# Kernel tuning notes

Hardware: AMD Instinct MI355X
Metric: run time of the kernel (lower is better)

The kernel has to match this reference:

```python
import jax, jax.numpy as jnp
import numpy as np

D_MODEL = 256
NHEAD = 8
HEAD_DIM = D_MODEL // NHEAD
LN_EPS = 1e-5
NEG_INF = -1e30  # finite large-negative; avoids NaN rows while matching masked softmax


def setup_inputs() -> dict:
    key = jax.random.key(0)
    ks = jax.random.split(key, 9)
    B, Q, HW, D = 8, 100, 16384, D_MODEL
    s = 0.02
    return {
        "query": jax.random.normal(ks[0], (B, Q, D), jnp.float32),
        "key_value": jax.random.normal(ks[1], (B, HW, D), jnp.float32),
        "attn_mask": jax.random.randint(ks[2], (B * NHEAD, Q, HW), 0, 2) == 1,  # True = attend
        "in_proj_weight": jax.random.normal(ks[3], (3 * D, D), jnp.float32) * s,
        "in_proj_bias": jax.random.normal(ks[4], (3 * D,), jnp.float32) * s,
        "out_proj_weight": jax.random.normal(ks[5], (D, D), jnp.float32) * s,
        "out_proj_bias": jax.random.normal(ks[6], (D,), jnp.float32) * s,
        "ln_weight": jnp.ones((D,), jnp.float32),
        "ln_bias": jnp.zeros((D,), jnp.float32),
    }


def _mha_masked(query, key_value, attn_mask, in_proj_weight, in_proj_bias,
                out_proj_weight, out_proj_bias):
    B, Q, D = query.shape
    HW = key_value.shape[1]
    Wq, Wk, Wv = jnp.split(in_proj_weight, 3, axis=0)
    bq, bk, bv = jnp.split(in_proj_bias, 3, axis=0)
    q = (query @ Wq.T + bq).reshape(B, Q, NHEAD, HEAD_DIM)
    k = (key_value @ Wk.T + bk).reshape(B, HW, NHEAD, HEAD_DIM)
    v = (key_value @ Wv.T + bv).reshape(B, HW, NHEAD, HEAD_DIM)
    scale = 1.0 / np.sqrt(HEAD_DIM).astype(np.float32)
    scores = jnp.einsum("bqhd,bkhd->bhqk", q, k) * scale  # (B, H, Q, HW)
    attend = attn_mask.reshape(B, NHEAD, Q, HW)  # True = attend
    scores = jnp.where(attend, scores, NEG_INF)
    probs = jax.nn.softmax(scores, axis=-1)
    ctx = jnp.einsum("bhqk,bkhd->bqhd", probs, v).reshape(B, Q, D)
    return ctx @ out_proj_weight.T + out_proj_bias


def reference(query, key_value, attn_mask, in_proj_weight, in_proj_bias,
              out_proj_weight, out_proj_bias, ln_weight, ln_bias):
    attn_out = _mha_masked(query, key_value, attn_mask, in_proj_weight,
                           in_proj_bias, out_proj_weight, out_proj_bias)
    x = query + attn_out  # dropout p=0.0 is identity
    mu = jnp.mean(x, axis=-1, keepdims=True)
    var = jnp.mean(jnp.square(x - mu), axis=-1, keepdims=True)
    return (x - mu) * jax.lax.rsqrt(var + LN_EPS) * ln_weight + ln_bias
```

## Files before the change

kernel.cpp:

```cpp
#include <hip/hip_runtime.h>
#include <stdint.h>

#define BB   8
#define NH   8
#define QQ   100
#define HWK  16384
#define DM   256
#define HD   32
#define QP   112
#define MT   7
#define NPART 64
#define SCALE2 0.2550602534365564f

typedef short bf16x8 __attribute__((ext_vector_type(8)));
typedef float f32x4  __attribute__((ext_vector_type(4)));
typedef unsigned short u16;
typedef unsigned int   u32;
typedef unsigned long long u64;

__device__ __forceinline__ u16 f2bf(float f) {
  u32 u = __builtin_bit_cast(u32, f);
  u += 0x7fffu + ((u >> 16) & 1u);
  return (u16)(u >> 16);
}
__device__ __forceinline__ u16 f2bf_ru(float f) {
  return (u16)((__builtin_bit_cast(u32, f) + 0x8000u) >> 16);
}
__device__ __forceinline__ u32 pack2rn(float lo, float hi) {
  u32 a = __builtin_bit_cast(u32, lo) + 0x8000u;
  u32 b = __builtin_bit_cast(u32, hi) + 0x8000u;
  return __builtin_amdgcn_perm(b, a, 0x07060302u);
}
__device__ __forceinline__ float bf_lo(u32 u) {
  return __builtin_bit_cast(float, u << 16);
}
__device__ __forceinline__ float bf_hi(u32 u) {
  return __builtin_bit_cast(float, u & 0xffff0000u);
}
__device__ __forceinline__ float fast_exp2(float x) {
#if __has_builtin(__builtin_amdgcn_exp2f)
  return __builtin_amdgcn_exp2f(x);
#else
  return exp2f(x);
#endif
}

__global__ __launch_bounds__(256) void wconv_kernel(
    const float* __restrict__ W, u16* __restrict__ wbf) {
  const int i = (blockIdx.x * 256 + threadIdx.x) * 4;
  const float4 w = *(const float4*)(W + 256 * DM + i);
  u32* dst = (u32*)(wbf + i);
  dst[0] = pack2rn(w.x, w.y);
  dst[1] = pack2rn(w.z, w.w);
}

__global__ __launch_bounds__(256) void proj_q_kernel(
    const float* __restrict__ query, const float* __restrict__ W,
    const float* __restrict__ bias, u16* __restrict__ q_bf) {
  __shared__ float xrow[DM];
  const int bq = blockIdx.x;
  const int b = bq / QQ, qi = bq % QQ;
  const int tid = threadIdx.x;
  if (tid < 64)
    ((float4*)xrow)[tid] = ((const float4*)(query + (size_t)bq * DM))[tid];
  __syncthreads();
  const int j = tid;
  float acc = bias[j];
  const float4* wr = (const float4*)(W + (size_t)j * DM);
  #pragma unroll 8
  for (int c = 0; c < 64; ++c) {
    float4 w = wr[c];
    float4 x = ((const float4*)xrow)[c];
    acc += w.x * x.x + w.y * x.y + w.z * x.z + w.w * x.w;
  }
  acc *= SCALE2;
  const int h = j >> 5, d = j & 31;
  q_bf[(((size_t)(b * NH + h)) * QQ + qi) * HD + d] = f2bf(acc);
}

__global__ __launch_bounds__(256) void proj_kv_kernel(
    const float* __restrict__ kv, const u16* __restrict__ wbf,
    const float* __restrict__ bias, u16* __restrict__ k_bf,
    u16* __restrict__ v_t) {
  __shared__ u16 Tl[4][5120];
  const int rb = blockIdx.x;
  const size_t m0 = (size_t)rb * 64;
  const int tid = threadIdx.x, lane = tid & 63, wid = tid >> 6;
  const int lane15 = lane & 15, quad = lane >> 4;
  const int jw = wid * 128;

  f32x4 acc[4][8];
  #pragma unroll
  for (int mi = 0; mi < 4; ++mi)
    #pragma unroll
    for (int ni = 0; ni < 8; ++ni) acc[mi][ni] = (f32x4){0.f, 0.f, 0.f, 0.f};

  for (int ks = 0; ks < 8; ++ks) {
    bf16x8 afr[4];
    #pragma unroll
    for (int mi = 0; mi < 4; ++mi) {
      const float* ap = kv + (m0 + mi * 16 + lane15) * DM + ks * 32 + quad * 8;
      float4 a0 = ((const float4*)ap)[0];
      float4 a1 = ((const float4*)ap)[1];
      uint4 w;
      w.x = pack2rn(a0.x, a0.y); w.y = pack2rn(a0.z, a0.w);
      w.z = pack2rn(a1.x, a1.y); w.w = pack2rn(a1.z, a1.w);
      afr[mi] = __builtin_bit_cast(bf16x8, w);
    }
    #pragma unroll
    for (int ni = 0; ni < 8; ++ni) {
      bf16x8 bfr = __builtin_bit_cast(bf16x8,
          *(const uint4*)(wbf + (size_t)(jw + ni * 16 + lane15) * DM + ks * 32 + quad * 8));
      #pragma unroll
      for (int mi = 0; mi < 4; ++mi)
        acc[mi][ni] = __builtin_amdgcn_mfma_f32_16x16x32_bf16(afr[mi], bfr, acc[mi][ni], 0, 0, 0);
    }
  }

  u16* T = Tl[wid];
  const float* bptr = bias + 256 + jw;
  if (wid < 2) {
    #pragma unroll
    for (int p = 0; p < 2; ++p) {
      #pragma unroll
      for (int mm = 0; mm < 2; ++mm) {
        const int mi = p * 2 + mm;
        #pragma unroll
        for (int ni = 0; ni < 8; ++ni) {
          const float bv = bptr[ni * 16 + lane15];
          #pragma unroll
          for (int r = 0; r < 4; ++r)
            T[(mm * 16 + quad * 4 + r) * 136 + ni * 16 + lane15] =
                f2bf_ru(acc[mi][ni][r] + bv);
        }
      }
      #pragma unroll
      for (int it = 0; it < 8; ++it) {
        const int row = it * 4 + quad;
        const int c0 = lane15 * 8;
        uint4 val = *(const uint4*)&T[row * 136 + c0];
        const size_t m = m0 + p * 32 + row;
        const size_t b = m >> 14, key = m & 16383;
        const int col256 = jw + c0;
        const int h = col256 >> 5, d = col256 & 31;
        *(uint4*)&k_bf[((b * NH + h) * HWK + key) * HD + d] = val;
      }
    }
  } else {
    const int jwv = jw - 256;
    #pragma unroll
    for (int p = 0; p < 2; ++p) {
      #pragma unroll
      for (int mm = 0; mm < 2; ++mm) {
        const int mi = p * 2 + mm;
        #pragma unroll
        for (int ni = 0; ni < 8; ++ni) {
          const float bv = bptr[ni * 16 + lane15];
          u32* dst = (u32*)&T[(ni * 16 + lane15) * 40 + mm * 16 + quad * 4];
          dst[0] = pack2rn(acc[mi][ni][0] + bv, acc[mi][ni][1] + bv);
          dst[1] = pack2rn(acc[mi][ni][2] + bv, acc[mi][ni][3] + bv);
        }
      }
      #pragma unroll
      for (int it = 0; it < 8; ++it) {
        const int col = it * 16 + (lane >> 2);
        const int koff = (lane & 3) * 8;
        uint4 val = *(const uint4*)&T[col * 40 + koff];
        const size_t m = m0 + p * 32 + koff;
        const size_t b = m >> 14, key = m & 16383;
        const int col256 = jwv + col;
        const int h = col256 >> 5, d = col256 & 31;
        *(uint4*)&v_t[((b * NH + h) * HD + d) * HWK + key] = val;
      }
    }
  }
}

__global__ __launch_bounds__(256) void attn_kernel(
    const u16* __restrict__ q_bf, const u16* __restrict__ k_bf,
    const u16* __restrict__ v_t, const int* __restrict__ mask,
    float* __restrict__ l_p, u32* __restrict__ ctxp) {
  __shared__ u16 qlds[QP * 40];
  __shared__ u32 mbitsw[QP * 33];
  const int tid = threadIdx.x;
  const int lane = tid & 63, wid = tid >> 6;
  const int lane15 = lane & 15, quad = lane >> 4;
  const int bh = blockIdx.x >> 4, chunk = blockIdx.x & 15;

  for (int i = tid; i < QP * HD; i += 256) {
    const int row = i >> 5, d = i & 31;
    qlds[row * 40 + d] = (row < QQ) ? q_bf[((size_t)bh * QQ + row) * HD + d] : (u16)0;
  }
  {
    const int* mp_base = mask + (size_t)bh * QQ * HWK + chunk * 1024;
    for (int rr = 0; rr < 25; ++rr) {
      const int row = wid * 25 + rr;
      const int* mp = mp_base + (size_t)row * HWK;
      u32 myw = 0;
      #pragma unroll
      for (int g = 0; g < 16; ++g) {
        const int mv = mp[g * 64 + lane];
        const u64 bl = __ballot(mv != 0);
        if (lane == 2 * g)     myw = (u32)bl;
        if (lane == 2 * g + 1) myw = (u32)(bl >> 32);
      }
      if (lane < 32) mbitsw[row * 33 + lane] = myw;
    }
  }
  __syncthreads();

  const int klocal_base = wid * 256;
  const int key_base = chunk * 1024 + klocal_base;
  const u16* kbase = k_bf + (size_t)bh * HWK * HD;
  const u16* vtb  = v_t  + (size_t)bh * HWK * HD;

  const int sl_lo = lane15 + 32 * (quad & 1);
  const int sl_hi = sl_lo + 16;
  const u32 selperm = (quad & 2) ? 0x07060302u : 0x05040100u;

  f32x4 acc[MT][2];
  float l_run[MT];
  #pragma unroll
  for (int mt = 0; mt < MT; ++mt) {
    acc[mt][0] = (f32x4){0.f, 0.f, 0.f, 0.f};
    acc[mt][1] = (f32x4){0.f, 0.f, 0.f, 0.f};
    l_run[mt] = 0.f;
  }

  for (int kg = 0; kg < 8; ++kg) {
    const int key0 = key_base + kg * 32;
    const int widx = wid * 8 + kg;
    bf16x8 kf0 = __builtin_bit_cast(bf16x8,
        *(const uint4*)(kbase + (size_t)(key0 + lane15) * HD + quad * 8));
    bf16x8 kf1 = __builtin_bit_cast(bf16x8,
        *(const uint4*)(kbase + (size_t)(key0 + 16 + lane15) * HD + quad * 8));
    bf16x8 vf0 = __builtin_bit_cast(bf16x8,
        *(const uint4*)(vtb + (size_t)lane15 * HWK + key0 + quad * 8));
    bf16x8 vf1 = __builtin_bit_cast(bf16x8,
        *(const uint4*)(vtb + (size_t)(lane15 + 16) * HWK + key0 + quad * 8));
    #pragma unroll
    for (int mt = 0; mt < MT; ++mt) {
      const int rowg = mt * 16 + lane15;
      bf16x8 af = __builtin_bit_cast(bf16x8,
          *(const uint4*)&qlds[rowg * 40 + quad * 8]);
      const f32x4 zero = {0.f, 0.f, 0.f, 0.f};
      f32x4 s0 = __builtin_amdgcn_mfma_f32_16x16x32_bf16(kf0, af, zero, 0, 0, 0);
      f32x4 s1 = __builtin_amdgcn_mfma_f32_16x16x32_bf16(kf1, af, zero, 0, 0, 0);
      u32 word = mbitsw[rowg * 33 + widx];
      if (rowg >= QQ) word = 0u;
      u32 pk[4];
      float lsum = 0.f;
      #pragma unroll
      for (int r = 0; r < 4; ++r) {
        const int kl = quad * 4 + r;
        const float p0 = ((word >> kl) & 1u)        ? fast_exp2(s0[r]) : 0.f;
        const float p1 = ((word >> (kl + 16)) & 1u) ? fast_exp2(s1[r]) : 0.f;
        lsum += p0 + p1;
        pk[r] = pack2rn(p0, p1);
      }
      l_run[mt] += lsum;
      u32 wA0 = (u32)__shfl((int)pk[0], sl_lo);
      u32 wA1 = (u32)__shfl((int)pk[1], sl_lo);
      u32 wA2 = (u32)__shfl((int)pk[2], sl_lo);
      u32 wA3 = (u32)__shfl((int)pk[3], sl_lo);
      u32 wB0 = (u32)__shfl((int)pk[0], sl_hi);
      u32 wB1 = (u32)__shfl((int)pk[1], sl_hi);
      u32 wB2 = (u32)__shfl((int)pk[2], sl_hi);
      u32 wB3 = (u32)__shfl((int)pk[3], sl_hi);
      uint4 pw;
      pw.x = __builtin_amdgcn_perm(wA1, wA0, selperm);
      pw.y = __builtin_amdgcn_perm(wA3, wA2, selperm);
      pw.z = __builtin_amdgcn_perm(wB1, wB0, selperm);
      pw.w = __builtin_amdgcn_perm(wB3, wB2, selperm);
      bf16x8 pf = __builtin_bit_cast(bf16x8, pw);
      acc[mt][0] = __builtin_amdgcn_mfma_f32_16x16x32_bf16(vf0, pf, acc[mt][0], 0, 0, 0);
      acc[mt][1] = __builtin_amdgcn_mfma_f32_16x16x32_bf16(vf1, pf, acc[mt][1], 0, 0, 0);
    }
  }

  const int part = chunk * 4 + wid;
  #pragma unroll
  for (int mt = 0; mt < MT; ++mt) {
    const int row = mt * 16 + lane15;
    float lr = l_run[mt];
    lr += __shfl_xor(lr, 16);
    lr += __shfl_xor(lr, 32);
    const size_t base = ((size_t)bh * QP + row) * NPART + part;
    if (quad == 0) l_p[base] = lr;
    uint2 lo2, hi2;
    lo2.x = pack2rn(acc[mt][0][0], acc[mt][0][1]);
    lo2.y = pack2rn(acc[mt][0][2], acc[mt][0][3]);
    hi2.x = pack2rn(acc[mt][1][0], acc[mt][1][1]);
    hi2.y = pack2rn(acc[mt][1][2], acc[mt][1][3]);
    *(uint2*)&ctxp[base * 16 + quad * 2]     = lo2;
    *(uint2*)&ctxp[base * 16 + 8 + quad * 2] = hi2;
  }
}

__global__ __launch_bounds__(256) void combine_kernel(
    const float* __restrict__ l_p, const u32* __restrict__ ctxp,
    const float* __restrict__ query, const float* __restrict__ Wo,
    const float* __restrict__ bo, const float* __restrict__ lnw,
    const float* __restrict__ lnb, float* __restrict__ out) {
  __shared__ float ctx_row[DM];
  __shared__ float red[8];
  const int bq = blockIdx.x;
  const int b = bq / QQ, qi = bq % QQ;
  const int tid = threadIdx.x, lane = tid & 63, wid = tid >> 6;

  for (int hh = 0; hh < 2; ++hh) {
    const int h = wid * 2 + hh;
    const size_t base = ((size_t)(b * NH + h) * QP + qi) * NPART;
    float lv = l_p[base + lane];
    #pragma unroll
    for (int o = 1; o < 64; o <<= 1) lv += __shfl_xor(lv, o);
    const float inv_l = 1.0f / lv;
    const int c = lane & 7, pg = lane >> 3;
    const u32* cp = ctxp + base * 16 + c * 2;
    float s0 = 0.f, s1 = 0.f, s2 = 0.f, s3 = 0.f;
    for (int p = pg; p < NPART; p += 8) {
      uint2 u = *(const uint2*)(cp + (size_t)p * 16);
      s0 += bf_lo(u.x); s1 += bf_hi(u.x);
      s2 += bf_lo(u.y); s3 += bf_hi(u.y);
    }
    #pragma unroll
    for (int o = 8; o < 64; o <<= 1) {
      s0 += __shfl_xor(s0, o);
      s1 += __shfl_xor(s1, o);
      s2 += __shfl_xor(s2, o);
      s3 += __shfl_xor(s3, o);
    }
    if (pg == 0) {
      ctx_row[h * HD + c * 4]     = s0 * inv_l;
      ctx_row[h * HD + c * 4 + 1] = s1 * inv_l;
      ctx_row[h * HD + c * 4 + 2] = s2 * inv_l;
      ctx_row[h * HD + c * 4 + 3] = s3 * inv_l;
    }
  }
  __syncthreads();

  const int j = tid;
  float s = bo[j];
  const float4* wr = (const float4*)(Wo + (size_t)j * DM);
  #pragma unroll 8
  for (int c = 0; c < 64; ++c) {
    float4 wv = wr[c];
    float4 cx = ((const float4*)ctx_row)[c];
    s += wv.x * cx.x + wv.y * cx.y + wv.z * cx.z + wv.w * cx.w;
  }
  const float x = s + query[(size_t)bq * DM + j];

  float t = x;
  #pragma unroll
  for (int o = 1; o < 64; o <<= 1) t += __shfl_xor(t, o);
  if (lane == 0) red[wid] = t;
  __syncthreads();
  const float mu = (red[0] + red[1] + red[2] + red[3]) * (1.0f / DM);
  const float dx = x - mu;
  float t2 = dx * dx;
  #pragma unroll
  for (int o = 1; o < 64; o <<= 1) t2 += __shfl_xor(t2, o);
  if (lane == 0) red[4 + wid] = t2;
  __syncthreads();
  const float var = (red[4] + red[5] + red[6] + red[7]) * (1.0f / DM);
  out[(size_t)bq * DM + j] = dx * rsqrtf(var + 1e-5f) * lnw[j] + lnb[j];
}

extern "C" void kernel_launch(void* const* d_in, const int* in_sizes, int n_in,
                              void* d_out, int out_size, void* d_ws, size_t ws_size,
                              hipStream_t stream) {
  const float* query = (const float*)d_in[0];
  const float* kv    = (const float*)d_in[1];
  const int*   mask  = (const int*)d_in[2];
  const float* ipw   = (const float*)d_in[3];
  const float* ipb   = (const float*)d_in[4];
  const float* opw   = (const float*)d_in[5];
  const float* opb   = (const float*)d_in[6];
  const float* lnw   = (const float*)d_in[7];
  const float* lnb   = (const float*)d_in[8];
  float* out = (float*)d_out;

  char* ws = (char*)d_ws;
  u16*   k_bf  = (u16*)(ws);
  u16*   v_t   = (u16*)(ws + 67108864);
  u16*   q_bf  = (u16*)(ws + 134217728);
  float* l_p   = (float*)(ws + 134742016);
  u32*   ctxp  = (u32*)(ws + 136577024);
  u16*   wbf   = (u16*)(ws + 195297280);

  wconv_kernel  <<<128,          256, 0, stream>>>(ipw, wbf);
  proj_q_kernel <<<BB * QQ,      256, 0, stream>>>(query, ipw, ipb, q_bf);
  proj_kv_kernel<<<2048,         256, 0, stream>>>(kv, wbf, ipb, k_bf, v_t);
  attn_kernel   <<<BB * NH * 16, 256, 0, stream>>>(q_bf, k_bf, v_t, mask, l_p, ctxp);
  combine_kernel<<<BB * QQ,      256, 0, stream>>>(l_p, ctxp, query, opw, opb, lnw, lnb, out);
}
```

Measured before the change: 868.4 us.

## Prefetch loads in projection and attention loops, fuse weight conversion, shrink KV tiles

```diff
diff --git a/kernel.cpp b/kernel.cpp
--- a/kernel.cpp
+++ b/kernel.cpp
@@ -45,22 +45,21 @@
 #endif
 }
 
-__global__ __launch_bounds__(256) void wconv_kernel(
-    const float* __restrict__ W, u16* __restrict__ wbf) {
-  const int i = (blockIdx.x * 256 + threadIdx.x) * 4;
-  const float4 w = *(const float4*)(W + 256 * DM + i);
-  u32* dst = (u32*)(wbf + i);
-  dst[0] = pack2rn(w.x, w.y);
-  dst[1] = pack2rn(w.z, w.w);
-}
-
 __global__ __launch_bounds__(256) void proj_q_kernel(
     const float* __restrict__ query, const float* __restrict__ W,
-    const float* __restrict__ bias, u16* __restrict__ q_bf) {
+    const float* __restrict__ bias, u16* __restrict__ q_bf,
+    u16* __restrict__ wbf) {
   __shared__ float xrow[DM];
   const int bq = blockIdx.x;
+  const int tid = threadIdx.x;
+  if (bq < 128) {
+    const int i = (bq * 256 + tid) * 4;
+    const float4 w = *(const float4*)(W + 256 * DM + i);
+    u32* dst = (u32*)(wbf + i);
+    dst[0] = pack2rn(w.x, w.y);
+    dst[1] = pack2rn(w.z, w.w);
+  }
   const int b = bq / QQ, qi = bq % QQ;
-  const int tid = threadIdx.x;
   if (tid < 64)
     ((float4*)xrow)[tid] = ((const float4*)(query + (size_t)bq * DM))[tid];
   __syncthreads();
@@ -78,33 +77,53 @@
   q_bf[(((size_t)(b * NH + h)) * QQ + qi) * HD + d] = f2bf(acc);
 }
 
-__global__ __launch_bounds__(256) void proj_kv_kernel(
+__global__ __launch_bounds__(256, 4) void proj_kv_kernel(
     const float* __restrict__ kv, const u16* __restrict__ wbf,
     const float* __restrict__ bias, u16* __restrict__ k_bf,
     u16* __restrict__ v_t) {
   __shared__ u16 Tl[4][5120];
   const int rb = blockIdx.x;
-  const size_t m0 = (size_t)rb * 64;
+  const size_t m0 = (size_t)rb * 32;
   const int tid = threadIdx.x, lane = tid & 63, wid = tid >> 6;
   const int lane15 = lane & 15, quad = lane >> 4;
   const int jw = wid * 128;
 
-  f32x4 acc[4][8];
-  #pragma unroll
-  for (int mi = 0; mi < 4; ++mi)
+  f32x4 acc[2][8];
+  #pragma unroll
+  for (int mi = 0; mi < 2; ++mi)
     #pragma unroll
     for (int ni = 0; ni < 8; ++ni) acc[mi][ni] = (f32x4){0.f, 0.f, 0.f, 0.f};
 
+  const float* abase = kv + (m0 + lane15) * DM + quad * 8;
+  float4 a_cur[2][2], a_nxt[2][2];
+  #pragma unroll
+  for (int mi = 0; mi < 2; ++mi) {
+    a_cur[mi][0] = ((const float4*)(abase + mi * 16 * DM))[0];
+    a_cur[mi][1] = ((const float4*)(abase + mi * 16 * DM))[1];
+  }
+
   for (int ks = 0; ks < 8; ++ks) {
-    bf16x8 afr[4];
-    #pragma unroll
-    for (int mi = 0; mi < 4; ++mi) {
-      const float* ap = kv + (m0 + mi * 16 + lane15) * DM + ks * 32 + quad * 8;
-      float4 a0 = ((const float4*)ap)[0];
-      float4 a1 = ((const float4*)ap)[1];
+    #pragma unroll
+    for (int mi = 0; mi < 2; ++mi) {
+      a_nxt[mi][0] = a_cur[mi][0];
+      a_nxt[mi][1] = a_cur[mi][1];
+    }
+    if (ks < 7) {
+      #pragma unroll
+      for (int mi = 0; mi < 2; ++mi) {
+        const float* ap = abase + mi * 16 * DM + (ks + 1) * 32;
+        a_nxt[mi][0] = ((const float4*)ap)[0];
+        a_nxt[mi][1] = ((const float4*)ap)[1];
+      }
+    }
+    bf16x8 afr[2];
+    #pragma unroll
+    for (int mi = 0; mi < 2; ++mi) {
       uint4 w;
-      w.x = pack2rn(a0.x, a0.y); w.y = pack2rn(a0.z, a0.w);
-      w.z = pack2rn(a1.x, a1.y); w.w = pack2rn(a1.z, a1.w);
+      w.x = pack2rn(a_cur[mi][0].x, a_cur[mi][0].y);
+      w.y = pack2rn(a_cur[mi][0].z, a_cur[mi][0].w);
+      w.z = pack2rn(a_cur[mi][1].x, a_cur[mi][1].y);
+      w.w = pack2rn(a_cur[mi][1].z, a_cur[mi][1].w);
       afr[mi] = __builtin_bit_cast(bf16x8, w);
     }
     #pragma unroll
@@ -112,8 +131,13 @@
       bf16x8 bfr = __builtin_bit_cast(bf16x8,
           *(const uint4*)(wbf + (size_t)(jw + ni * 16 + lane15) * DM + ks * 32 + quad * 8));
       #pragma unroll
-      for (int mi = 0; mi < 4; ++mi)
+      for (int mi = 0; mi < 2; ++mi)
         acc[mi][ni] = __builtin_amdgcn_mfma_f32_16x16x32_bf16(afr[mi], bfr, acc[mi][ni], 0, 0, 0);
+    }
+    #pragma unroll
+    for (int mi = 0; mi < 2; ++mi) {
+      a_cur[mi][0] = a_nxt[mi][0];
+      a_cur[mi][1] = a_nxt[mi][1];
     }
   }
 
@@ -121,62 +145,54 @@
   const float* bptr = bias + 256 + jw;
   if (wid < 2) {
     #pragma unroll
-    for (int p = 0; p < 2; ++p) {
-      #pragma unroll
-      for (int mm = 0; mm < 2; ++mm) {
-        const int mi = p * 2 + mm;
+    for (int mi = 0; mi < 2; ++mi) {
+      #pragma unroll
+      for (int ni = 0; ni < 8; ++ni) {
+        const float bv = bptr[ni * 16 + lane15];
         #pragma unroll
-        for (int ni = 0; ni < 8; ++ni) {
-          const float bv = bptr[ni * 16 + lane15];
-          #pragma unroll
-          for (int r = 0; r < 4; ++r)
-            T[(mm * 16 + quad * 4 + r) * 136 + ni * 16 + lane15] =
-                f2bf_ru(acc[mi][ni][r] + bv);
-        }
-      }
-      #pragma unroll
-      for (int it = 0; it < 8; ++it) {
-        const int row = it * 4 + quad;
-        const int c0 = lane15 * 8;
-        uint4 val = *(const uint4*)&T[row * 136 + c0];
-        const size_t m = m0 + p * 32 + row;
-        const size_t b = m >> 14, key = m & 16383;
-        const int col256 = jw + c0;
-        const int h = col256 >> 5, d = col256 & 31;
-        *(uint4*)&k_bf[((b * NH + h) * HWK + key) * HD + d] = val;
-      }
+        for (int r = 0; r < 4; ++r)
+          T[(mi * 16 + quad * 4 + r) * 136 + ni * 16 + lane15] =
+              f2bf_ru(acc[mi][ni][r] + bv);
+      }
+    }
+    #pragma unroll
+    for (int it = 0; it < 8; ++it) {
+      const int row = it * 4 + quad;
+      const int c0 = lane15 * 8;
+      uint4 val = *(const uint4*)&T[row * 136 + c0];
+      const size_t m = m0 + row;
+      const size_t b = m >> 14, key = m & 16383;
+      const int col256 = jw + c0;
+      const int h = col256 >> 5, d = col256 & 31;
+      *(uint4*)&k_bf[((b * NH + h) * HWK + key) * HD + d] = val;
     }
   } else {
     const int jwv = jw - 256;
     #pragma unroll
-    for (int p = 0; p < 2; ++p) {
-      #pragma unroll
-      for (int mm = 0; mm < 2; ++mm) {
-        const int mi = p * 2 + mm;
-        #pragma unroll
-        for (int ni = 0; ni < 8; ++ni) {
-          const float bv = bptr[ni * 16 + lane15];
-          u32* dst = (u32*)&T[(ni * 16 + lane15) * 40 + mm * 16 + quad * 4];
-          dst[0] = pack2rn(acc[mi][ni][0] + bv, acc[mi][ni][1] + bv);
-          dst[1] = pack2rn(acc[mi][ni][2] + bv, acc[mi][ni][3] + bv);
-        }
-      }
-      #pragma unroll
-      for (int it = 0; it < 8; ++it) {
-        const int col = it * 16 + (lane >> 2);
-        const int koff = (lane & 3) * 8;
-        uint4 val = *(const uint4*)&T[col * 40 + koff];
-        const size_t m = m0 + p * 32 + koff;
-        const size_t b = m >> 14, key = m & 16383;
-        const int col256 = jwv + col;
-        const int h = col256 >> 5, d = col256 & 31;
-        *(uint4*)&v_t[((b * NH + h) * HD + d) * HWK + key] = val;
-      }
-    }
-  }
-}
-
-__global__ __launch_bounds__(256) void attn_kernel(
+    for (int mi = 0; mi < 2; ++mi) {
+      #pragma unroll
+      for (int ni = 0; ni < 8; ++ni) {
+        const float bv = bptr[ni * 16 + lane15];
+        u32* dst = (u32*)&T[(ni * 16 + lane15) * 40 + mi * 16 + quad * 4];
+        dst[0] = pack2rn(acc[mi][ni][0] + bv, acc[mi][ni][1] + bv);
+        dst[1] = pack2rn(acc[mi][ni][2] + bv, acc[mi][ni][3] + bv);
+      }
+    }
+    #pragma unroll
+    for (int it = 0; it < 8; ++it) {
+      const int col = it * 16 + (lane >> 2);
+      const int koff = (lane & 3) * 8;
+      uint4 val = *(const uint4*)&T[col * 40 + koff];
+      const size_t m = m0 + koff;
+      const size_t b = m >> 14, key = m & 16383;
+      const int col256 = jwv + col;
+      const int h = col256 >> 5, d = col256 & 31;
+      *(uint4*)&v_t[((b * NH + h) * HD + d) * HWK + key] = val;
+    }
+  }
+}
+
+__global__ __launch_bounds__(256, 3) void attn_kernel(
     const u16* __restrict__ q_bf, const u16* __restrict__ k_bf,
     const u16* __restrict__ v_t, const int* __restrict__ mask,
     float* __restrict__ l_p, u32* __restrict__ ctxp) {
@@ -192,19 +208,27 @@
     qlds[row * 40 + d] = (row < QQ) ? q_bf[((size_t)bh * QQ + row) * HD + d] : (u16)0;
   }
   {
-    const int* mp_base = mask + (size_t)bh * QQ * HWK + chunk * 1024;
+    const int* mp_base = mask + (size_t)bh * QQ * HWK + chunk * 1024
+                         + (size_t)(wid * 25) * HWK;
+    int cur[16], nxt[16];
+    #pragma unroll
+    for (int g = 0; g < 16; ++g) cur[g] = mp_base[g * 64 + lane];
     for (int rr = 0; rr < 25; ++rr) {
-      const int row = wid * 25 + rr;
-      const int* mp = mp_base + (size_t)row * HWK;
+      if (rr < 24) {
+        const int* mp = mp_base + (size_t)(rr + 1) * HWK;
+        #pragma unroll
+        for (int g = 0; g < 16; ++g) nxt[g] = mp[g * 64 + lane];
+      }
       u32 myw = 0;
       #pragma unroll
       for (int g = 0; g < 16; ++g) {
-        const int mv = mp[g * 64 + lane];
-        const u64 bl = __ballot(mv != 0);
+        const u64 bl = __ballot(cur[g] != 0);
         if (lane == 2 * g)     myw = (u32)bl;
         if (lane == 2 * g + 1) myw = (u32)(bl >> 32);
       }
-      if (lane < 32) mbitsw[row * 33 + lane] = myw;
+      if (lane < 32) mbitsw[(wid * 25 + rr) * 33 + lane] = myw;
+      #pragma unroll
+      for (int g = 0; g < 16; ++g) cur[g] = nxt[g];
     }
   }
   __syncthreads();
@@ -227,27 +251,40 @@
     l_run[mt] = 0.f;
   }
 
+  uint4 kr0 = *(const uint4*)(kbase + (size_t)(key_base + lane15) * HD + quad * 8);
+  uint4 kr1 = *(const uint4*)(kbase + (size_t)(key_base + 16 + lane15) * HD + quad * 8);
+  uint4 vr0 = *(const uint4*)(vtb + (size_t)lane15 * HWK + key_base + quad * 8);
+  uint4 vr1 = *(const uint4*)(vtb + (size_t)(lane15 + 16) * HWK + key_base + quad * 8);
+
   for (int kg = 0; kg < 8; ++kg) {
-    const int key0 = key_base + kg * 32;
+    uint4 nk0 = kr0, nk1 = kr1, nv0 = vr0, nv1 = vr1;
+    if (kg < 7) {
+      const int key0n = key_base + (kg + 1) * 32;
+      nk0 = *(const uint4*)(kbase + (size_t)(key0n + lane15) * HD + quad * 8);
+      nk1 = *(const uint4*)(kbase + (size_t)(key0n + 16 + lane15) * HD + quad * 8);
+      nv0 = *(const uint4*)(vtb + (size_t)lane15 * HWK + key0n + quad * 8);
+      nv1 = *(const uint4*)(vtb + (size_t)(lane15 + 16) * HWK + key0n + quad * 8);
+    }
     const int widx = wid * 8 + kg;
-    bf16x8 kf0 = __builtin_bit_cast(bf16x8,
-        *(const uint4*)(kbase + (size_t)(key0 + lane15) * HD + quad * 8));
-    bf16x8 kf1 = __builtin_bit_cast(bf16x8,
-        *(const uint4*)(kbase + (size_t)(key0 + 16 + lane15) * HD + quad * 8));
-    bf16x8 vf0 = __builtin_bit_cast(bf16x8,
-        *(const uint4*)(vtb + (size_t)lane15 * HWK + key0 + quad * 8));
-    bf16x8 vf1 = __builtin_bit_cast(bf16x8,
-        *(const uint4*)(vtb + (size_t)(lane15 + 16) * HWK + key0 + quad * 8));
+    u32 wm[MT];
     #pragma unroll
     for (int mt = 0; mt < MT; ++mt) {
       const int rowg = mt * 16 + lane15;
+      wm[mt] = mbitsw[rowg * 33 + widx];
+      if (rowg >= QQ) wm[mt] = 0u;
+    }
+    bf16x8 kf0 = __builtin_bit_cast(bf16x8, kr0);
+    bf16x8 kf1 = __builtin_bit_cast(bf16x8, kr1);
+    bf16x8 vf0 = __builtin_bit_cast(bf16x8, vr0);
+    bf16x8 vf1 = __builtin_bit_cast(bf16x8, vr1);
+    #pragma unroll
+    for (int mt = 0; mt < MT; ++mt) {
       bf16x8 af = __builtin_bit_cast(bf16x8,
-          *(const uint4*)&qlds[rowg * 40 + quad * 8]);
+          *(const uint4*)&qlds[(mt * 16 + lane15) * 40 + quad * 8]);
       const f32x4 zero = {0.f, 0.f, 0.f, 0.f};
       f32x4 s0 = __builtin_amdgcn_mfma_f32_16x16x32_bf16(kf0, af, zero, 0, 0, 0);
       f32x4 s1 = __builtin_amdgcn_mfma_f32_16x16x32_bf16(kf1, af, zero, 0, 0, 0);
-      u32 word = mbitsw[rowg * 33 + widx];
-      if (rowg >= QQ) word = 0u;
+      const u32 word = wm[mt];
       u32 pk[4];
       float lsum = 0.f;
       #pragma unroll
@@ -276,6 +313,7 @@
       acc[mt][0] = __builtin_amdgcn_mfma_f32_16x16x32_bf16(vf0, pf, acc[mt][0], 0, 0, 0);
       acc[mt][1] = __builtin_amdgcn_mfma_f32_16x16x32_bf16(vf1, pf, acc[mt][1], 0, 0, 0);
     }
+    kr0 = nk0; kr1 = nk1; vr0 = nv0; vr1 = nv1;
   }
 
   const int part = chunk * 4 + wid;
@@ -388,9 +426,8 @@
   u32*   ctxp  = (u32*)(ws + 136577024);
   u16*   wbf   = (u16*)(ws + 195297280);
 
-  wconv_kernel  <<<128,          256, 0, stream>>>(ipw, wbf);
-  proj_q_kernel <<<BB * QQ,      256, 0, stream>>>(query, ipw, ipb, q_bf);
-  proj_kv_kernel<<<2048,         256, 0, stream>>>(kv, wbf, ipb, k_bf, v_t);
+  proj_q_kernel <<<BB * QQ,      256, 0, stream>>>(query, ipw, ipb, q_bf, wbf);
+  proj_kv_kernel<<<4096,         256, 0, stream>>>(kv, wbf, ipb, k_bf, v_t);
   attn_kernel   <<<BB * NH * 16, 256, 0, stream>>>(q_bf, k_bf, v_t, mask, l_p, ctxp);
   combine_kernel<<<BB * QQ,      256, 0, stream>>>(l_p, ctxp, query, opw, opb, lnw, lnb, out);
 }
```

Result: slower. 982.5 us (+13.1%).
